# Kernel tuning notes

Hardware: AMD Instinct MI355X
Metric: run time of the kernel (lower is better)

## Reference

```python
import jax, jax.numpy as jnp
import numpy as np

B, S, D, H, HD, FF, V = 256, 512, 128, 4, 32, 512, 256
THRESHOLD = 4.0


def _ln(x, g, b, eps=1e-5):
    m = x.mean(-1, keepdims=True)
    v = jnp.var(x, axis=-1, keepdims=True)  # biased var, matches torch LayerNorm
    return (x - m) / jnp.sqrt(v + eps) * g + b


def setup_inputs() -> dict:
    key = jax.random.key(0)
    ks = jax.random.split(key, 10)
    g = lambda i, shape: jax.random.normal(ks[i], shape, jnp.float32) * 0.05
    return {
        "input_bytes": jax.random.randint(ks[0], (B, S), 0, V, jnp.int32),
        "emb": g(1, (V, D)),
        "pos_emb": g(2, (S, D)),
        "ln_g": jnp.ones((D,), jnp.float32), "ln_b": jnp.zeros((D,), jnp.float32),
        "attn_w": g(3, (2, 3 * D, D)), "attn_b": jnp.zeros((2, 3 * D), jnp.float32),
        "out_w": g(4, (2, D, D)), "out_b": jnp.zeros((2, D), jnp.float32),
        "ff1_w": g(5, (2, FF, D)), "ff1_b": jnp.zeros((2, FF), jnp.float32),
        "ff2_w": g(6, (2, D, FF)), "ff2_b": jnp.zeros((2, D), jnp.float32),
        "n1_g": jnp.ones((2, D), jnp.float32), "n1_b": jnp.zeros((2, D), jnp.float32),
        "n2_g": jnp.ones((2, D), jnp.float32), "n2_b": jnp.zeros((2, D), jnp.float32),
        "proj_w": g(7, (V, D)), "proj_b": jnp.zeros((V,), jnp.float32),
    }


def _avg_entropy(input_bytes, emb, pos_emb, ln_g, ln_b, attn_w, attn_b, out_w,
                 out_b, ff1_w, ff1_b, ff2_w, ff2_b, n1_g, n1_b, n2_g, n2_b,
                 proj_w, proj_b):
    h = emb[input_bytes] + pos_emb[None, :, :]          # [B,S,D]
    h = _ln(h, ln_g, ln_b)
    scale = jnp.asarray(1.0 / np.sqrt(HD), jnp.float32)
    for l in range(2):  # post-norm TransformerEncoderLayer, relu FFN
        qkv = h @ attn_w[l].T + attn_b[l]               # [B,S,3D]
        q, k, v = jnp.split(qkv, 3, axis=-1)
        q = q.reshape(B, S, H, HD)
        k = k.reshape(B, S, H, HD)
        v = v.reshape(B, S, H, HD)
        scores = jnp.einsum('bqhd,bkhd->bhqk', q, k) * scale
        a = jax.nn.softmax(scores, axis=-1)
        o = jnp.einsum('bhqk,bkhd->bqhd', a, v).reshape(B, S, D)
        o = o @ out_w[l].T + out_b[l]
        h = _ln(h + o, n1_g[l], n1_b[l])
        f = jax.nn.relu(h @ ff1_w[l].T + ff1_b[l]) @ ff2_w[l].T + ff2_b[l]
        h = _ln(h + f, n2_g[l], n2_b[l])
    logits = h @ proj_w.T + proj_b                      # [B,S,256]
    probs = jax.nn.softmax(logits, axis=-1)
    entropy = -jnp.sum(probs * jnp.log(probs + 1e-10), axis=-1)  # [B,S]
    return entropy.mean(axis=0)                         # [S]


def reference(input_bytes, emb, pos_emb, ln_g, ln_b, attn_w, attn_b, out_w,
              out_b, ff1_w, ff1_b, ff2_w, ff2_b, n1_g, n1_b, n2_g, n2_b,
              proj_w, proj_b):
    avg_entropy = _avg_entropy(input_bytes, emb, pos_emb, ln_g, ln_b, attn_w,
                               attn_b, out_w, out_b, ff1_w, ff1_b, ff2_w,
                               ff2_b, n1_g, n1_b, n2_g, n2_b, proj_w, proj_b)
    # Fixed-shape form of the entropy-threshold patch segmentation:
    # boundary[i]=1 iff a new patch starts at i (i>=1 and avg_entropy[i]>thr).
    boundary = jnp.concatenate([
        jnp.zeros((1,), jnp.int32),
        (avg_entropy[1:] > THRESHOLD).astype(jnp.int32),
    ])
    segment_ids = jnp.cumsum(boundary)                  # patch id per position
    return avg_entropy, segment_ids
```

## Files before the change

### kernel.cpp

```cpp
#include <hip/hip_runtime.h>


typedef __bf16 bf16x8 __attribute__((ext_vector_type(8)));
typedef float  f32x4  __attribute__((ext_vector_type(4)));

__device__ __forceinline__ unsigned short f2bf(float f) {
  union { float f; unsigned int u; } c; c.f = f;
  unsigned int u = c.u;
  u += 0x7FFFu + ((u >> 16) & 1u);
  return (unsigned short)(u >> 16);
}
__device__ __forceinline__ float bf2f(unsigned short u) {
  union { unsigned int u; float f; } c; c.u = ((unsigned int)u) << 16;
  return c.f;
}

__device__ __forceinline__ float EXP2(float x) {
#if __has_builtin(__builtin_amdgcn_exp2f)
  return __builtin_amdgcn_exp2f(x);
#else
  return exp2f(x);
#endif
}

__device__ __forceinline__ unsigned int cvtpk_bf16(float lo, float hi) {
  unsigned int r;
  asm("v_cvt_pk_bf16_f32 %0, %1, %2" : "=v"(r) : "v"(lo), "v"(hi));
  return r;
}
__device__ __forceinline__ void plswap32(unsigned int& a, unsigned int& b) {
  asm("v_permlane32_swap_b32 %0, %1" : "+v"(a), "+v"(b));
}
__device__ __forceinline__ void plswap16(unsigned int& a, unsigned int& b) {
  asm("v_permlane16_swap_b32 %0, %1" : "+v"(a), "+v"(b));
}
__device__ __forceinline__ bf16x8 packfrag(f32x4 a, f32x4 b) {
  unsigned int w00 = cvtpk_bf16(a[0], a[1]), w01 = cvtpk_bf16(a[2], a[3]);
  unsigned int w10 = cvtpk_bf16(b[0], b[1]), w11 = cvtpk_bf16(b[2], b[3]);
  plswap32(w00, w10); plswap16(w00, w10);
  plswap32(w01, w11); plswap16(w01, w11);
  union { unsigned int u[4]; bf16x8 v; } pk;
  pk.u[0] = w00; pk.u[1] = w01; pk.u[2] = w10; pk.u[3] = w11;
  return pk.v;
}

#define MFMA __builtin_amdgcn_mfma_f32_16x16x32_bf16

__global__ void conv_permA(const float* __restrict__ src,
                           unsigned short* __restrict__ dst, int K, int n) {
  int i = blockIdx.x * 256 + threadIdx.x;
  if (i >= n) return;
  int row = i / K, k = i - row * K;
  int frag = (row >> 4) * (K >> 5) + (k >> 5);
  int d = frag * 512 + ((k >> 3) & 3) * 128 + (row & 15) * 8 + (k & 7);
  dst[d] = f2bf(src[i]);
}

#define QSCALE 0.2550602989892646f
__global__ void conv_attn_headA(const float* __restrict__ src,
                                unsigned short* __restrict__ dst) {
  int i = blockIdx.x * 256 + threadIdx.x;
  int l = i / 49152, rem = i - l * 49152;
  int row = rem >> 7, k = rem & 127;
  int mat = row >> 7;
  int head = (row >> 5) & 3;
  int dr = row & 31;
  float v = src[i];
  if (mat == 0) v *= QSCALE;
  int d = ((l * 4 + head) * 3 + mat) * 4096 +
          ((dr >> 4) * 4 + (k >> 5)) * 512 + ((k >> 3) & 3) * 128 +
          (dr & 15) * 8 + (k & 7);
  dst[d] = f2bf(v);
}
__global__ void conv_attn_b(const float* __restrict__ src,
                            float* __restrict__ dst) {
  int i = blockIdx.x * 256 + threadIdx.x;
  if (i < 768) {
    float v = src[i];
    if ((i % 384) < 128) v *= QSCALE;
    dst[i] = v;
  }
}

__global__ __launch_bounds__(256) void embed_ln(
    const int* __restrict__ bytes, const float* __restrict__ emb,
    const float* __restrict__ pos, const float* __restrict__ g,
    const float* __restrict__ bta, unsigned short* __restrict__ hbf) {
  int wv = threadIdx.x >> 6, lane = threadIdx.x & 63;
  int tok = blockIdx.x * 4 + wv;
  int s = tok & 511;
  int bidx = bytes[tok];
  const float* e = emb + (size_t)bidx * 128;
  const float* p = pos + (size_t)s * 128;
  float x0 = e[lane] + p[lane];
  float x1 = e[lane + 64] + p[lane + 64];
  float sum = x0 + x1, ssq = x0 * x0 + x1 * x1;
#pragma unroll
  for (int off = 32; off; off >>= 1) {
    sum += __shfl_xor(sum, off);
    ssq += __shfl_xor(ssq, off);
  }
  float mean = sum * 0.0078125f;
  float var = ssq * 0.0078125f - mean * mean;
  float rs = rsqrtf(var + 1e-5f);
  float y0 = (x0 - mean) * rs * g[lane] + bta[lane];
  float y1 = (x1 - mean) * rs * g[lane + 64] + bta[lane + 64];
  size_t o = (size_t)tok * 128;
  hbf[o + lane] = f2bf(y0); hbf[o + lane + 64] = f2bf(y1);
}

__global__ __launch_bounds__(512)
__attribute__((amdgpu_waves_per_eu(4, 4))) void attn_fused(
    const unsigned short* __restrict__ h, const unsigned short* __restrict__ Wa,
    const float* __restrict__ ab, unsigned short* __restrict__ obf) {
  __shared__ __bf16 Ks[32 * 512];
  __shared__ __bf16 Vt[32 * 512];

  const int hh = blockIdx.x & 3, bl = blockIdx.x >> 2;
  const int t = threadIdx.x;
  const int lane = t & 63, wv = t >> 6;
  const int c = lane & 15, g = lane >> 4;
  const size_t tok0 = (size_t)bl * 512;
  const size_t myq = tok0 + wv * 64;

  const unsigned short* Wb = Wa + hh * 3 * 4096;
  const float* bq = ab + hh * 32;
  const float* bk = ab + 128 + hh * 32;
  const float* bv = ab + 256 + hh * 32;

  bf16x8 qb[4];
  f32x4 dv[2][2];
#pragma unroll
  for (int tf = 0; tf < 4; ++tf) {
    bf16x8 a4[4];
#pragma unroll
    for (int kk = 0; kk < 4; ++kk)
      a4[kk] =
          *(const bf16x8*)(h + (myq + tf * 16 + c) * 128 + kk * 32 + g * 8);
    {
      f32x4 d0 = {}, d1 = {};
#pragma unroll
      for (int kk = 0; kk < 4; ++kk) {
        d0 = MFMA(*(const bf16x8*)(Wb + kk * 512 + lane * 8), a4[kk], d0,
                  0, 0, 0);
        d1 = MFMA(*(const bf16x8*)(Wb + (4 + kk) * 512 + lane * 8), a4[kk],
                  d1, 0, 0, 0);
      }
      float4 b0 = *(const float4*)(bq + g * 4);
      float4 b1 = *(const float4*)(bq + 16 + g * 4);
      d0[0] += b0.x; d0[1] += b0.y; d0[2] += b0.z; d0[3] += b0.w;
      d1[0] += b1.x; d1[1] += b1.y; d1[2] += b1.z; d1[3] += b1.w;
      qb[tf] = packfrag(d0, d1);
    }
    {
      f32x4 d0 = {}, d1 = {};
#pragma unroll
      for (int kk = 0; kk < 4; ++kk) {
        d0 = MFMA(*(const bf16x8*)(Wb + 4096 + kk * 512 + lane * 8), a4[kk],
                  d0, 0, 0, 0);
        d1 = MFMA(*(const bf16x8*)(Wb + 4096 + (4 + kk) * 512 + lane * 8),
                  a4[kk], d1, 0, 0, 0);
      }
      float4 b0 = *(const float4*)(bk + g * 4);
      float4 b1 = *(const float4*)(bk + 16 + g * 4);
      d0[0] += b0.x; d0[1] += b0.y; d0[2] += b0.z; d0[3] += b0.w;
      d1[0] += b1.x; d1[1] += b1.y; d1[2] += b1.z; d1[3] += b1.w;
      *(bf16x8*)&Ks[(wv * 4 + tf) * 512 + lane * 8] = packfrag(d0, d1);
    }
#pragma unroll
    for (int hf = 0; hf < 2; ++hf) {
      f32x4 tv = {};
#pragma unroll
      for (int kk = 0; kk < 4; ++kk)
        tv = MFMA(a4[kk],
                  *(const bf16x8*)(Wb + 8192 + (hf * 4 + kk) * 512 + lane * 8),
                  tv, 0, 0, 0);
      float bvv = bv[hf * 16 + c];
      tv[0] += bvv; tv[1] += bvv; tv[2] += bvv; tv[3] += bvv;
      dv[tf & 1][hf] = tv;
    }
    if (tf & 1) {
#pragma unroll
      for (int hf = 0; hf < 2; ++hf)
        *(bf16x8*)&Vt[(hf * 16 + wv * 2 + (tf >> 1)) * 512 + lane * 8] =
            packfrag(dv[0][hf], dv[1][hf]);
    }
  }
  __syncthreads();

  f32x4 ot[4][2] = {};
  float l[4] = {0.f, 0.f, 0.f, 0.f};
  const f32x4 zz = {0.f, 0.f, 0.f, 0.f};

  for (int kt = 0; kt < 8; ++kt) {
    bf16x8 ka[4];
#pragma unroll
    for (int kf = 0; kf < 4; ++kf)
      ka[kf] = *(const bf16x8*)&Ks[(kt * 4 + kf) * 512 + lane * 8];
    bf16x8 vb2[2][2];
#pragma unroll
    for (int hf = 0; hf < 2; ++hf)
#pragma unroll
      for (int ksl = 0; ksl < 2; ++ksl)
        vb2[hf][ksl] =
            *(const bf16x8*)&Vt[(hf * 16 + kt * 2 + ksl) * 512 + lane * 8];

#pragma unroll
    for (int qf = 0; qf < 4; ++qf) {
      f32x4 sA = MFMA(ka[0], qb[qf], zz, 0, 0, 0);
      f32x4 sB = MFMA(ka[1], qb[qf], zz, 0, 0, 0);
      f32x4 sC = MFMA(ka[2], qb[qf], zz, 0, 0, 0);
      f32x4 sD = MFMA(ka[3], qb[qf], zz, 0, 0, 0);

      {
        float pa0 = EXP2(sA[0]), pa1 = EXP2(sA[1]);
        float pa2 = EXP2(sA[2]), pa3 = EXP2(sA[3]);
        float pb0 = EXP2(sB[0]), pb1 = EXP2(sB[1]);
        float pb2 = EXP2(sB[2]), pb3 = EXP2(sB[3]);
        l[qf] += ((pa0 + pa1) + (pa2 + pa3)) + ((pb0 + pb1) + (pb2 + pb3));
        f32x4 pa = {pa0, pa1, pa2, pa3};
        f32x4 pb = {pb0, pb1, pb2, pb3};
        bf16x8 pk = packfrag(pa, pb);
        ot[qf][0] = MFMA(vb2[0][0], pk, ot[qf][0], 0, 0, 0);
        ot[qf][1] = MFMA(vb2[1][0], pk, ot[qf][1], 0, 0, 0);
      }
      {
        float pa0 = EXP2(sC[0]), pa1 = EXP2(sC[1]);
        float pa2 = EXP2(sC[2]), pa3 = EXP2(sC[3]);
        float pb0 = EXP2(sD[0]), pb1 = EXP2(sD[1]);
        float pb2 = EXP2(sD[2]), pb3 = EXP2(sD[3]);
        l[qf] += ((pa0 + pa1) + (pa2 + pa3)) + ((pb0 + pb1) + (pb2 + pb3));
        f32x4 pa = {pa0, pa1, pa2, pa3};
        f32x4 pb = {pb0, pb1, pb2, pb3};
        bf16x8 pk = packfrag(pa, pb);
        ot[qf][0] = MFMA(vb2[0][1], pk, ot[qf][0], 0, 0, 0);
        ot[qf][1] = MFMA(vb2[1][1], pk, ot[qf][1], 0, 0, 0);
      }
    }
  }

#pragma unroll
  for (int qf = 0; qf < 4; ++qf) {
    l[qf] += __shfl_xor(l[qf], 16);
    l[qf] += __shfl_xor(l[qf], 32);
  }
#pragma unroll
  for (int qf = 0; qf < 4; ++qf) {
    float rl = 1.0f / l[qf];
#pragma unroll
    for (int hf = 0; hf < 2; ++hf) {
      ushort4 pk;
      pk.x = f2bf(ot[qf][hf][0] * rl);
      pk.y = f2bf(ot[qf][hf][1] * rl);
      pk.z = f2bf(ot[qf][hf][2] * rl);
      pk.w = f2bf(ot[qf][hf][3] * rl);
      *(ushort4*)(obf + (myq + qf * 16 + c) * 128 + hh * 32 + hf * 16 +
                  g * 4) = pk;
    }
  }
}

__global__ __launch_bounds__(256) void oproj_ln(
    const unsigned short* __restrict__ A, const unsigned short* __restrict__ Wp,
    const float* __restrict__ bias, unsigned short* __restrict__ h,
    const float* __restrict__ gamma, const float* __restrict__ beta) {
  const int lane = threadIdx.x & 63, w = threadIdx.x >> 6;
  const int c = lane & 15, g = lane >> 4;
  const size_t tok0 = (size_t)blockIdx.x * 128 + w * 32;

  bf16x8 at[2][4];
#pragma unroll
  for (int tf = 0; tf < 2; ++tf)
#pragma unroll
    for (int kk = 0; kk < 4; ++kk)
      at[tf][kk] =
          *(const bf16x8*)(A + (tok0 + tf * 16 + c) * 128 + kk * 32 + g * 8);

  f32x4 acc[8][2] = {};
#pragma unroll
  for (int db = 0; db < 8; ++db)
#pragma unroll
    for (int kk = 0; kk < 4; ++kk) {
      bf16x8 wf = *(const bf16x8*)(Wp + (db * 4 + kk) * 512 + lane * 8);
      acc[db][0] = MFMA(wf, at[0][kk], acc[db][0], 0, 0, 0);
      acc[db][1] = MFMA(wf, at[1][kk], acc[db][1], 0, 0, 0);
    }

#pragma unroll
  for (int tf = 0; tf < 2; ++tf) {
    unsigned short* hrow = h + (tok0 + tf * 16 + c) * 128;
    float x[8][4];
    float s_ = 0.f, q_ = 0.f;
#pragma unroll
    for (int db = 0; db < 8; ++db) {
      float4 bvv = *(const float4*)(bias + db * 16 + g * 4);
      ushort4 rv = *(const ushort4*)(hrow + db * 16 + g * 4);
      x[db][0] = acc[db][tf][0] + bvv.x + bf2f(rv.x);
      x[db][1] = acc[db][tf][1] + bvv.y + bf2f(rv.y);
      x[db][2] = acc[db][tf][2] + bvv.z + bf2f(rv.z);
      x[db][3] = acc[db][tf][3] + bvv.w + bf2f(rv.w);
#pragma unroll
      for (int r = 0; r < 4; ++r) { s_ += x[db][r]; q_ += x[db][r] * x[db][r]; }
    }
    s_ += __shfl_xor(s_, 16); s_ += __shfl_xor(s_, 32);
    q_ += __shfl_xor(q_, 16); q_ += __shfl_xor(q_, 32);
    float mean = s_ * 0.0078125f;
    float var = q_ * 0.0078125f - mean * mean;
    float rs = rsqrtf(var + 1e-5f);
#pragma unroll
    for (int db = 0; db < 8; ++db) {
      float4 gv = *(const float4*)(gamma + db * 16 + g * 4);
      float4 bb = *(const float4*)(beta + db * 16 + g * 4);
      ushort4 o;
      o.x = f2bf((x[db][0] - mean) * rs * gv.x + bb.x);
      o.y = f2bf((x[db][1] - mean) * rs * gv.y + bb.y);
      o.z = f2bf((x[db][2] - mean) * rs * gv.z + bb.z);
      o.w = f2bf((x[db][3] - mean) * rs * gv.w + bb.w);
      *(ushort4*)(hrow + db * 16 + g * 4) = o;
    }
  }
}

__global__ __launch_bounds__(256) void ffn_reg(
    unsigned short* __restrict__ h, const unsigned short* __restrict__ W1p,
    const float* __restrict__ b1, const unsigned short* __restrict__ W2p,
    const float* __restrict__ b2, const float* __restrict__ gamma,
    const float* __restrict__ beta) {
  const int lane = threadIdx.x & 63, w = threadIdx.x >> 6;
  const int c = lane & 15, g = lane >> 4;
  const size_t tok0 = (size_t)blockIdx.x * 128 + w * 32;

  bf16x8 at[2][4];
#pragma unroll
  for (int tf = 0; tf < 2; ++tf)
#pragma unroll
    for (int kk = 0; kk < 4; ++kk)
      at[tf][kk] =
          *(const bf16x8*)(h + (tok0 + tf * 16 + c) * 128 + kk * 32 + g * 8);

  f32x4 acc[8][2] = {};
  for (int s = 0; s < 16; ++s) {
    f32x4 d1[2][2] = {};
#pragma unroll
    for (int kk = 0; kk < 4; ++kk) {
      bf16x8 wa = *(const bf16x8*)(W1p + ((2 * s) * 4 + kk) * 512 + lane * 8);
      bf16x8 wb = *(const bf16x8*)(W1p + ((2 * s + 1) * 4 + kk) * 512 + lane * 8);
      d1[0][0] = MFMA(wa, at[0][kk], d1[0][0], 0, 0, 0);
      d1[0][1] = MFMA(wa, at[1][kk], d1[0][1], 0, 0, 0);
      d1[1][0] = MFMA(wb, at[0][kk], d1[1][0], 0, 0, 0);
      d1[1][1] = MFMA(wb, at[1][kk], d1[1][1], 0, 0, 0);
    }
    float4 bva = *(const float4*)(b1 + s * 32 + g * 4);
    float4 bvb = *(const float4*)(b1 + s * 32 + 16 + g * 4);
    bf16x8 gp[2];
#pragma unroll
    for (int tf = 0; tf < 2; ++tf) {
      f32x4 pa, pb;
      pa[0] = fmaxf(d1[0][tf][0] + bva.x, 0.f);
      pa[1] = fmaxf(d1[0][tf][1] + bva.y, 0.f);
      pa[2] = fmaxf(d1[0][tf][2] + bva.z, 0.f);
      pa[3] = fmaxf(d1[0][tf][3] + bva.w, 0.f);
      pb[0] = fmaxf(d1[1][tf][0] + bvb.x, 0.f);
      pb[1] = fmaxf(d1[1][tf][1] + bvb.y, 0.f);
      pb[2] = fmaxf(d1[1][tf][2] + bvb.z, 0.f);
      pb[3] = fmaxf(d1[1][tf][3] + bvb.w, 0.f);
      gp[tf] = packfrag(pa, pb);
    }
#pragma unroll
    for (int db = 0; db < 8; ++db) {
      bf16x8 w2 = *(const bf16x8*)(W2p + (db * 16 + s) * 512 + lane * 8);
      acc[db][0] = MFMA(w2, gp[0], acc[db][0], 0, 0, 0);
      acc[db][1] = MFMA(w2, gp[1], acc[db][1], 0, 0, 0);
    }
  }

#pragma unroll
  for (int tf = 0; tf < 2; ++tf) {
    unsigned short* hrow = h + (tok0 + tf * 16 + c) * 128;
    float x[8][4];
    float s_ = 0.f, q_ = 0.f;
#pragma unroll
    for (int db = 0; db < 8; ++db) {
      float4 bvv = *(const float4*)(b2 + db * 16 + g * 4);
      ushort4 rv = *(const ushort4*)(hrow + db * 16 + g * 4);
      x[db][0] = acc[db][tf][0] + bvv.x + bf2f(rv.x);
      x[db][1] = acc[db][tf][1] + bvv.y + bf2f(rv.y);
      x[db][2] = acc[db][tf][2] + bvv.z + bf2f(rv.z);
      x[db][3] = acc[db][tf][3] + bvv.w + bf2f(rv.w);
#pragma unroll
      for (int r = 0; r < 4; ++r) { s_ += x[db][r]; q_ += x[db][r] * x[db][r]; }
    }
    s_ += __shfl_xor(s_, 16); s_ += __shfl_xor(s_, 32);
    q_ += __shfl_xor(q_, 16); q_ += __shfl_xor(q_, 32);
    float mean = s_ * 0.0078125f;
    float var = q_ * 0.0078125f - mean * mean;
    float rs = rsqrtf(var + 1e-5f);
#pragma unroll
    for (int db = 0; db < 8; ++db) {
      float4 gv = *(const float4*)(gamma + db * 16 + g * 4);
      float4 bb = *(const float4*)(beta + db * 16 + g * 4);
      ushort4 o;
      o.x = f2bf((x[db][0] - mean) * rs * gv.x + bb.x);
      o.y = f2bf((x[db][1] - mean) * rs * gv.y + bb.y);
      o.z = f2bf((x[db][2] - mean) * rs * gv.z + bb.z);
      o.w = f2bf((x[db][3] - mean) * rs * gv.w + bb.w);
      *(ushort4*)(hrow + db * 16 + g * 4) = o;
    }
  }
}

__global__ __launch_bounds__(256) void vocab_entropy(
    const unsigned short* __restrict__ h, const unsigned short* __restrict__ Wp,
    const float* __restrict__ bias, float* __restrict__ ent) {
  const int lane = threadIdx.x & 63, w = threadIdx.x >> 6;
  const int c = lane & 15, g = lane >> 4;
  const size_t tok0 = (size_t)blockIdx.x * 128 + w * 32;

  bf16x8 at[2][4];
#pragma unroll
  for (int tf = 0; tf < 2; ++tf)
#pragma unroll
    for (int kk = 0; kk < 4; ++kk)
      at[tf][kk] =
          *(const bf16x8*)(h + (tok0 + tf * 16 + c) * 128 + kk * 32 + g * 8);

  f32x4 acc[16][2] = {};
#pragma unroll
  for (int vb = 0; vb < 16; ++vb)
#pragma unroll
    for (int kk = 0; kk < 4; ++kk) {
      bf16x8 wf = *(const bf16x8*)(Wp + (vb * 4 + kk) * 512 + lane * 8);
      acc[vb][0] = MFMA(wf, at[0][kk], acc[vb][0], 0, 0, 0);
      acc[vb][1] = MFMA(wf, at[1][kk], acc[vb][1], 0, 0, 0);
    }

  const float L2E = 1.4426950408889634f;
#pragma unroll
  for (int tf = 0; tf < 2; ++tf) {
    float m_ = -1e30f;
#pragma unroll
    for (int vb = 0; vb < 16; ++vb) {
      float4 bvv = *(const float4*)(bias + vb * 16 + g * 4);
      acc[vb][tf][0] += bvv.x; acc[vb][tf][1] += bvv.y;
      acc[vb][tf][2] += bvv.z; acc[vb][tf][3] += bvv.w;
      m_ = fmaxf(m_, fmaxf(fmaxf(acc[vb][tf][0], acc[vb][tf][1]),
                           fmaxf(acc[vb][tf][2], acc[vb][tf][3])));
    }
    m_ = fmaxf(m_, __shfl_xor(m_, 16));
    m_ = fmaxf(m_, __shfl_xor(m_, 32));
    float z_ = 0.f, sx_ = 0.f;
#pragma unroll
    for (int vb = 0; vb < 16; ++vb)
#pragma unroll
      for (int r = 0; r < 4; ++r) {
        float xx = acc[vb][tf][r];
        float e = EXP2((xx - m_) * L2E);
        z_ += e; sx_ += e * xx;
      }
    z_ += __shfl_xor(z_, 16);  z_ += __shfl_xor(z_, 32);
    sx_ += __shfl_xor(sx_, 16); sx_ += __shfl_xor(sx_, 32);
    if (g == 0) ent[tok0 + tf * 16 + c] = m_ + logf(z_) - sx_ / z_;
  }
}

__global__ __launch_bounds__(64) void avg_entropy_kernel(
    const float* __restrict__ ent, float* __restrict__ out) {
  int s = blockIdx.x, lane = threadIdx.x;
  float a = 0.f;
  for (int b = lane; b < 256; b += 64) a += ent[(size_t)b * 512 + s];
#pragma unroll
  for (int off = 32; off; off >>= 1) a += __shfl_xor(a, off);
  if (lane == 0) out[s] = a * 0.00390625f;
}

__global__ __launch_bounds__(512) void seg_kernel(float* out) {
  __shared__ int cs[512];
  int i = threadIdx.x;
  float e = out[i];
  cs[i] = (i >= 1 && e > 4.0f) ? 1 : 0;
  __syncthreads();
  for (int off = 1; off < 512; off <<= 1) {
    int v = (i >= off) ? cs[i - off] : 0;
    __syncthreads();
    cs[i] += v;
    __syncthreads();
  }
  out[512 + i] = (float)cs[i];
}

extern "C" void kernel_launch(void* const* d_in, const int* in_sizes, int n_in,
                              void* d_out, int out_size, void* d_ws,
                              size_t ws_size, hipStream_t stream) {
  (void)in_sizes; (void)n_in; (void)out_size; (void)ws_size;
  const int*   input_bytes = (const int*)d_in[0];
  const float* emb    = (const float*)d_in[1];
  const float* pos    = (const float*)d_in[2];
  const float* ln_g   = (const float*)d_in[3];
  const float* ln_b   = (const float*)d_in[4];
  const float* attn_w = (const float*)d_in[5];
  const float* attn_b = (const float*)d_in[6];
  const float* out_w  = (const float*)d_in[7];
  const float* out_b  = (const float*)d_in[8];
  const float* ff1_w  = (const float*)d_in[9];
  const float* ff1_b  = (const float*)d_in[10];
  const float* ff2_w  = (const float*)d_in[11];
  const float* ff2_b  = (const float*)d_in[12];
  const float* n1_g   = (const float*)d_in[13];
  const float* n1_b   = (const float*)d_in[14];
  const float* n2_g   = (const float*)d_in[15];
  const float* n2_b   = (const float*)d_in[16];
  const float* proj_w = (const float*)d_in[17];
  const float* proj_b = (const float*)d_in[18];

  char* ws = (char*)d_ws;
  unsigned short* hbf  = (unsigned short*)(ws);
  unsigned short* obf  = (unsigned short*)(ws + 33554432);
  unsigned short* wbf  = (unsigned short*)(ws + 67108864);
  float*          absb = (float*)(ws + 68157440);
  float*          entb = (float*)(ws + 68161536);

  unsigned short* attnA = wbf;
  unsigned short* outwA = wbf + 98304;
  unsigned short* w1A   = wbf + 131072;
  unsigned short* w2A   = wbf + 262144;
  unsigned short* projA = wbf + 393216;

  conv_attn_headA<<<384, 256, 0, stream>>>(attn_w, attnA);
  conv_attn_b<<<3, 256, 0, stream>>>(attn_b, absb);
  for (int l = 0; l < 2; ++l) {
    conv_permA<<<64, 256, 0, stream>>>(out_w + l * 16384, outwA + l * 16384,
                                       128, 16384);
    conv_permA<<<256, 256, 0, stream>>>(ff1_w + l * 65536, w1A + l * 65536,
                                        128, 65536);
    conv_permA<<<256, 256, 0, stream>>>(ff2_w + l * 65536, w2A + l * 65536,
                                        512, 65536);
  }
  conv_permA<<<128, 256, 0, stream>>>(proj_w, projA, 128, 32768);

  embed_ln<<<32768, 256, 0, stream>>>(input_bytes, emb, pos, ln_g, ln_b, hbf);

  for (int l = 0; l < 2; ++l) {
    attn_fused<<<1024, 512, 0, stream>>>(hbf, attnA + l * 49152,
                                         absb + l * 384, obf);
    oproj_ln<<<1024, 256, 0, stream>>>(obf, outwA + l * 16384, out_b + l * 128,
                                       hbf, n1_g + l * 128, n1_b + l * 128);
    ffn_reg<<<1024, 256, 0, stream>>>(hbf, w1A + l * 65536, ff1_b + l * 512,
                                      w2A + l * 65536, ff2_b + l * 128,
                                      n2_g + l * 128, n2_b + l * 128);
  }

  vocab_entropy<<<1024, 256, 0, stream>>>(hbf, projA, proj_b, entb);
  avg_entropy_kernel<<<512, 64, 0, stream>>>(entb, (float*)d_out);
  seg_kernel<<<1, 512, 0, stream>>>((float*)d_out);
}
```

Baseline: 433.2 us.

## Fuse out-projection LN and FFN into one kernel; add MFMA priority hints in attention

Merges the oproj_ln and ffn_reg kernels into a single block_tail kernel. The post-attention layernorm output stays in registers as the FFN's A operand and as its residual, so the intermediate h no longer makes a global round trip and one launch per layer goes away. The kernel also adds s_setprio around the MFMA groups in the attention loop to favour matrix issue over the exp work. In exchange, register pressure rises under launch_bounds(256,3), which may cause spills or lower occupancy. The residual is now taken from a bf16-packed copy held in registers.

```diff
diff --git a/kernel.cpp b/kernel.cpp
--- a/kernel.cpp
+++ b/kernel.cpp
@@ -207,10 +207,12 @@
 
 #pragma unroll
     for (int qf = 0; qf < 4; ++qf) {
+      __builtin_amdgcn_s_setprio(1);
       f32x4 sA = MFMA(ka[0], qb[qf], zz, 0, 0, 0);
       f32x4 sB = MFMA(ka[1], qb[qf], zz, 0, 0, 0);
       f32x4 sC = MFMA(ka[2], qb[qf], zz, 0, 0, 0);
       f32x4 sD = MFMA(ka[3], qb[qf], zz, 0, 0, 0);
+      __builtin_amdgcn_s_setprio(0);
 
       {
         float pa0 = EXP2(sA[0]), pa1 = EXP2(sA[1]);
@@ -221,8 +223,10 @@
         f32x4 pa = {pa0, pa1, pa2, pa3};
         f32x4 pb = {pb0, pb1, pb2, pb3};
         bf16x8 pk = packfrag(pa, pb);
+        __builtin_amdgcn_s_setprio(1);
         ot[qf][0] = MFMA(vb2[0][0], pk, ot[qf][0], 0, 0, 0);
         ot[qf][1] = MFMA(vb2[1][0], pk, ot[qf][1], 0, 0, 0);
+        __builtin_amdgcn_s_setprio(0);
       }
       {
         float pa0 = EXP2(sC[0]), pa1 = EXP2(sC[1]);
@@ -233,8 +237,10 @@
         f32x4 pa = {pa0, pa1, pa2, pa3};
         f32x4 pb = {pb0, pb1, pb2, pb3};
         bf16x8 pk = packfrag(pa, pb);
+        __builtin_amdgcn_s_setprio(1);
         ot[qf][0] = MFMA(vb2[0][1], pk, ot[qf][0], 0, 0, 0);
         ot[qf][1] = MFMA(vb2[1][1], pk, ot[qf][1], 0, 0, 0);
+        __builtin_amdgcn_s_setprio(0);
       }
     }
   }
@@ -260,40 +266,47 @@
   }
 }
 
-__global__ __launch_bounds__(256) void oproj_ln(
-    const unsigned short* __restrict__ A, const unsigned short* __restrict__ Wp,
-    const float* __restrict__ bias, unsigned short* __restrict__ h,
-    const float* __restrict__ gamma, const float* __restrict__ beta) {
+__global__ __launch_bounds__(256, 3) void block_tail(
+    const unsigned short* __restrict__ A,
+    const unsigned short* __restrict__ Wo, const float* __restrict__ bo,
+    const float* __restrict__ g1, const float* __restrict__ b1n,
+    const unsigned short* __restrict__ W1p, const float* __restrict__ b1,
+    const unsigned short* __restrict__ W2p, const float* __restrict__ b2,
+    const float* __restrict__ g2, const float* __restrict__ b2n,
+    unsigned short* __restrict__ h) {
   const int lane = threadIdx.x & 63, w = threadIdx.x >> 6;
   const int c = lane & 15, g = lane >> 4;
   const size_t tok0 = (size_t)blockIdx.x * 128 + w * 32;
 
-  bf16x8 at[2][4];
-#pragma unroll
-  for (int tf = 0; tf < 2; ++tf)
-#pragma unroll
-    for (int kk = 0; kk < 4; ++kk)
-      at[tf][kk] =
-          *(const bf16x8*)(A + (tok0 + tf * 16 + c) * 128 + kk * 32 + g * 8);
-
   f32x4 acc[8][2] = {};
-#pragma unroll
-  for (int db = 0; db < 8; ++db)
-#pragma unroll
-    for (int kk = 0; kk < 4; ++kk) {
-      bf16x8 wf = *(const bf16x8*)(Wp + (db * 4 + kk) * 512 + lane * 8);
-      acc[db][0] = MFMA(wf, at[0][kk], acc[db][0], 0, 0, 0);
-      acc[db][1] = MFMA(wf, at[1][kk], acc[db][1], 0, 0, 0);
-    }
-
+  {
+    bf16x8 at[2][4];
+#pragma unroll
+    for (int tf = 0; tf < 2; ++tf)
+#pragma unroll
+      for (int kk = 0; kk < 4; ++kk)
+        at[tf][kk] =
+            *(const bf16x8*)(A + (tok0 + tf * 16 + c) * 128 + kk * 32 + g * 8);
+#pragma unroll
+    for (int db = 0; db < 8; ++db)
+#pragma unroll
+      for (int kk = 0; kk < 4; ++kk) {
+        bf16x8 wf = *(const bf16x8*)(Wo + (db * 4 + kk) * 512 + lane * 8);
+        acc[db][0] = MFMA(wf, at[0][kk], acc[db][0], 0, 0, 0);
+        acc[db][1] = MFMA(wf, at[1][kk], acc[db][1], 0, 0, 0);
+      }
+  }
+
+  unsigned int ybf[2][8][2];
+  bf16x8 at2[2][4];
 #pragma unroll
   for (int tf = 0; tf < 2; ++tf) {
-    unsigned short* hrow = h + (tok0 + tf * 16 + c) * 128;
+    const unsigned short* hrow = h + (tok0 + tf * 16 + c) * 128;
     float x[8][4];
     float s_ = 0.f, q_ = 0.f;
 #pragma unroll
     for (int db = 0; db < 8; ++db) {
-      float4 bvv = *(const float4*)(bias + db * 16 + g * 4);
+      float4 bvv = *(const float4*)(bo + db * 16 + g * 4);
       ushort4 rv = *(const ushort4*)(hrow + db * 16 + g * 4);
       x[db][0] = acc[db][tf][0] + bvv.x + bf2f(rv.x);
       x[db][1] = acc[db][tf][1] + bvv.y + bf2f(rv.y);
@@ -307,48 +320,34 @@
     float mean = s_ * 0.0078125f;
     float var = q_ * 0.0078125f - mean * mean;
     float rs = rsqrtf(var + 1e-5f);
+    f32x4 yv[8];
 #pragma unroll
     for (int db = 0; db < 8; ++db) {
-      float4 gv = *(const float4*)(gamma + db * 16 + g * 4);
-      float4 bb = *(const float4*)(beta + db * 16 + g * 4);
-      ushort4 o;
-      o.x = f2bf((x[db][0] - mean) * rs * gv.x + bb.x);
-      o.y = f2bf((x[db][1] - mean) * rs * gv.y + bb.y);
-      o.z = f2bf((x[db][2] - mean) * rs * gv.z + bb.z);
-      o.w = f2bf((x[db][3] - mean) * rs * gv.w + bb.w);
-      *(ushort4*)(hrow + db * 16 + g * 4) = o;
-    }
-  }
-}
-
-__global__ __launch_bounds__(256) void ffn_reg(
-    unsigned short* __restrict__ h, const unsigned short* __restrict__ W1p,
-    const float* __restrict__ b1, const unsigned short* __restrict__ W2p,
-    const float* __restrict__ b2, const float* __restrict__ gamma,
-    const float* __restrict__ beta) {
-  const int lane = threadIdx.x & 63, w = threadIdx.x >> 6;
-  const int c = lane & 15, g = lane >> 4;
-  const size_t tok0 = (size_t)blockIdx.x * 128 + w * 32;
-
-  bf16x8 at[2][4];
-#pragma unroll
-  for (int tf = 0; tf < 2; ++tf)
-#pragma unroll
-    for (int kk = 0; kk < 4; ++kk)
-      at[tf][kk] =
-          *(const bf16x8*)(h + (tok0 + tf * 16 + c) * 128 + kk * 32 + g * 8);
-
-  f32x4 acc[8][2] = {};
+      float4 gv = *(const float4*)(g1 + db * 16 + g * 4);
+      float4 bb = *(const float4*)(b1n + db * 16 + g * 4);
+      yv[db][0] = (x[db][0] - mean) * rs * gv.x + bb.x;
+      yv[db][1] = (x[db][1] - mean) * rs * gv.y + bb.y;
+      yv[db][2] = (x[db][2] - mean) * rs * gv.z + bb.z;
+      yv[db][3] = (x[db][3] - mean) * rs * gv.w + bb.w;
+      ybf[tf][db][0] = cvtpk_bf16(yv[db][0], yv[db][1]);
+      ybf[tf][db][1] = cvtpk_bf16(yv[db][2], yv[db][3]);
+    }
+#pragma unroll
+    for (int kb = 0; kb < 4; ++kb)
+      at2[tf][kb] = packfrag(yv[2 * kb], yv[2 * kb + 1]);
+  }
+
+  f32x4 acc2[8][2] = {};
   for (int s = 0; s < 16; ++s) {
     f32x4 d1[2][2] = {};
 #pragma unroll
     for (int kk = 0; kk < 4; ++kk) {
       bf16x8 wa = *(const bf16x8*)(W1p + ((2 * s) * 4 + kk) * 512 + lane * 8);
       bf16x8 wb = *(const bf16x8*)(W1p + ((2 * s + 1) * 4 + kk) * 512 + lane * 8);
-      d1[0][0] = MFMA(wa, at[0][kk], d1[0][0], 0, 0, 0);
-      d1[0][1] = MFMA(wa, at[1][kk], d1[0][1], 0, 0, 0);
-      d1[1][0] = MFMA(wb, at[0][kk], d1[1][0], 0, 0, 0);
-      d1[1][1] = MFMA(wb, at[1][kk], d1[1][1], 0, 0, 0);
+      d1[0][0] = MFMA(wa, at2[0][kk], d1[0][0], 0, 0, 0);
+      d1[0][1] = MFMA(wa, at2[1][kk], d1[0][1], 0, 0, 0);
+      d1[1][0] = MFMA(wb, at2[0][kk], d1[1][0], 0, 0, 0);
+      d1[1][1] = MFMA(wb, at2[1][kk], d1[1][1], 0, 0, 0);
     }
     float4 bva = *(const float4*)(b1 + s * 32 + g * 4);
     float4 bvb = *(const float4*)(b1 + s * 32 + 16 + g * 4);
@@ -369,8 +368,8 @@
 #pragma unroll
     for (int db = 0; db < 8; ++db) {
       bf16x8 w2 = *(const bf16x8*)(W2p + (db * 16 + s) * 512 + lane * 8);
-      acc[db][0] = MFMA(w2, gp[0], acc[db][0], 0, 0, 0);
-      acc[db][1] = MFMA(w2, gp[1], acc[db][1], 0, 0, 0);
+      acc2[db][0] = MFMA(w2, gp[0], acc2[db][0], 0, 0, 0);
+      acc2[db][1] = MFMA(w2, gp[1], acc2[db][1], 0, 0, 0);
     }
   }
 
@@ -382,11 +381,11 @@
 #pragma unroll
     for (int db = 0; db < 8; ++db) {
       float4 bvv = *(const float4*)(b2 + db * 16 + g * 4);
-      ushort4 rv = *(const ushort4*)(hrow + db * 16 + g * 4);
-      x[db][0] = acc[db][tf][0] + bvv.x + bf2f(rv.x);
-      x[db][1] = acc[db][tf][1] + bvv.y + bf2f(rv.y);
-      x[db][2] = acc[db][tf][2] + bvv.z + bf2f(rv.z);
-      x[db][3] = acc[db][tf][3] + bvv.w + bf2f(rv.w);
+      unsigned int y01 = ybf[tf][db][0], y23 = ybf[tf][db][1];
+      x[db][0] = acc2[db][tf][0] + bvv.x + bf2f((unsigned short)y01);
+      x[db][1] = acc2[db][tf][1] + bvv.y + bf2f((unsigned short)(y01 >> 16));
+      x[db][2] = acc2[db][tf][2] + bvv.z + bf2f((unsigned short)y23);
+      x[db][3] = acc2[db][tf][3] + bvv.w + bf2f((unsigned short)(y23 >> 16));
 #pragma unroll
       for (int r = 0; r < 4; ++r) { s_ += x[db][r]; q_ += x[db][r] * x[db][r]; }
     }
@@ -397,8 +396,8 @@
     float rs = rsqrtf(var + 1e-5f);
 #pragma unroll
     for (int db = 0; db < 8; ++db) {
-      float4 gv = *(const float4*)(gamma + db * 16 + g * 4);
-      float4 bb = *(const float4*)(beta + db * 16 + g * 4);
+      float4 gv = *(const float4*)(g2 + db * 16 + g * 4);
+      float4 bb = *(const float4*)(b2n + db * 16 + g * 4);
       ushort4 o;
       o.x = f2bf((x[db][0] - mean) * rs * gv.x + bb.x);
       o.y = f2bf((x[db][1] - mean) * rs * gv.y + bb.y);
@@ -542,11 +541,10 @@
   for (int l = 0; l < 2; ++l) {
     attn_fused<<<1024, 512, 0, stream>>>(hbf, attnA + l * 49152,
                                          absb + l * 384, obf);
-    oproj_ln<<<1024, 256, 0, stream>>>(obf, outwA + l * 16384, out_b + l * 128,
-                                       hbf, n1_g + l * 128, n1_b + l * 128);
-    ffn_reg<<<1024, 256, 0, stream>>>(hbf, w1A + l * 65536, ff1_b + l * 512,
-                                      w2A + l * 65536, ff2_b + l * 128,
-                                      n2_g + l * 128, n2_b + l * 128);
+    block_tail<<<1024, 256, 0, stream>>>(
+        obf, outwA + l * 16384, out_b + l * 128, n1_g + l * 128,
+        n1_b + l * 128, w1A + l * 65536, ff1_b + l * 512, w2A + l * 65536,
+        ff2_b + l * 128, n2_g + l * 128, n2_b + l * 128, hbf);
   }
 
   vocab_entropy<<<1024, 256, 0, stream>>>(hbf, projA, proj_b, entb);
```

Result: slower. 513.0 us (+18.4%).
